# Performance work log

Hardware: AMD Instinct MI355X
Metric: run time of the kernel (lower is better)

Reference implementation:

```python
import jax, jax.numpy as jnp
import numpy as np

NUM_HEADS = 32
HEAD_DIM = 128
NUM_KV_HEADS = 8
SCALE = 0.08838834764831845  # 1/sqrt(128)
SEQ_LEN = 2048
TOTAL_TOKENS = 4096  # batch=2 sequences of 2048


def setup_inputs() -> dict:
    key = jax.random.key(0)
    kq, kk, kv = jax.random.split(key, 3)
    q = jax.random.normal(kq, (TOTAL_TOKENS, NUM_HEADS * HEAD_DIM), dtype=jnp.float32)
    k = jax.random.normal(kk, (TOTAL_TOKENS, NUM_KV_HEADS * HEAD_DIM), dtype=jnp.float32)
    v = jax.random.normal(kv, (TOTAL_TOKENS, NUM_KV_HEADS * HEAD_DIM), dtype=jnp.float32)
    return {"q": q, "k": k, "v": v, "seq_len": SEQ_LEN}


def reference(q, k, v, seq_len):
    # Unified (varlen) causal GQA attention: flattened tokens are split into
    # batch sequences of equal length (the prefill path of the unified kernel).
    T = q.shape[0]
    B = T // seq_len
    G = NUM_HEADS // NUM_KV_HEADS  # query heads per kv head
    # [B, S, Hkv, G, D] and [B, S, Hkv, D]
    qh = q.reshape(B, seq_len, NUM_KV_HEADS, G, HEAD_DIM)
    kh = k.reshape(B, seq_len, NUM_KV_HEADS, HEAD_DIM)
    vh = v.reshape(B, seq_len, NUM_KV_HEADS, HEAD_DIM)
    # scores: [B, Hkv, G, Sq, Sk]
    scores = jnp.einsum("bqhgd,bkhd->bhgqk", qh, kh) * SCALE
    causal = jnp.tril(jnp.ones((seq_len, seq_len), dtype=bool))
    scores = jnp.where(causal, scores, jnp.finfo(scores.dtype).min)
    probs = jax.nn.softmax(scores, axis=-1)
    # out: [B, Sq, Hkv, G, D]
    o = jnp.einsum("bhgqk,bkhd->bqhgd", probs, vh)
    return o.reshape(T, NUM_HEADS * HEAD_DIM)
```

## Files before the change

kernel.cpp:

```cpp
#include <hip/hip_runtime.h>
#include <stdint.h>
#include <stddef.h>


#define S_LEN   2048
#define HQ      32
#define HKV     8
#define DH      128
#define QSTRIDE (HQ*DH)
#define KSTRIDE (HKV*DH)
#define SCALE_L2 0.12751139830213113f

#define KTILE      64
#define NTILES     (S_LEN/KTILE)
#define CSTRIDE    520
#define KPART      (16*CSTRIDE)
#define TILE_ELEMS (KPART + 16*CSTRIDE)

typedef __bf16 bf16;
typedef short        s16x4 __attribute__((ext_vector_type(4)));
typedef short        s16x8 __attribute__((ext_vector_type(8)));
typedef float        f32x4 __attribute__((ext_vector_type(4)));
typedef unsigned int u32x2 __attribute__((ext_vector_type(2)));
typedef unsigned int u32x4 __attribute__((ext_vector_type(4)));

__device__ __forceinline__ unsigned int pk2(float a, float b) {
  union { bf16 h[2]; unsigned int u; } x;
  x.h[0] = (bf16)a; x.h[1] = (bf16)b;
  return x.u;
}

__device__ __forceinline__ int koff(int chunk, int key) {
  return chunk*CSTRIDE + key*8;
}
__device__ __forceinline__ int voff(int unit, int d) {
  return KPART + unit*CSTRIDE + d*4;
}

__global__ __launch_bounds__(512, 4)
void attn_fwd(const float* __restrict__ qg, const float* __restrict__ kg,
              const float* __restrict__ vg, float* __restrict__ og) {
  __shared__ bf16 smem[2*TILE_ELEMS];

  const int tid   = threadIdx.x;
  const int lane  = tid & 63;
  const int wave  = tid >> 6;
  const int l15   = lane & 15;
  const int quad  = lane >> 4;
  const int pairp = blockIdx.x;
  const int h     = blockIdx.y;
  const int b     = blockIdx.z;
  const int hkv   = h >> 2;

  const int fk_key = tid >> 3, fk_cg = tid & 7;
  const int fv_u   = tid & 15, fv_dq = tid >> 4;
  float4 fkx[4], fvx[4];

  auto load_regs = [&](int t) {
    const float* kp = kg + (size_t)(b*S_LEN + t*KTILE + fk_key)*KSTRIDE
                         + hkv*DH + fk_cg*16;
#pragma unroll
    for (int i = 0; i < 4; ++i) fkx[i] = ((const float4*)kp)[i];
    const int d0 = fv_dq*4;
#pragma unroll
    for (int j = 0; j < 4; ++j)
      fvx[j] = *(const float4*)(vg + (size_t)(b*S_LEN + t*KTILE + fv_u*4 + j)*KSTRIDE
                                   + hkv*DH + d0);
  };
  auto store_tile = [&](int bi) {
    bf16* kb = smem + bi*TILE_ELEMS;
#pragma unroll
    for (int ii = 0; ii < 2; ++ii) {
      u32x4 w;
      w[0] = pk2(fkx[2*ii].x,   fkx[2*ii].y);   w[1] = pk2(fkx[2*ii].z,   fkx[2*ii].w);
      w[2] = pk2(fkx[2*ii+1].x, fkx[2*ii+1].y); w[3] = pk2(fkx[2*ii+1].z, fkx[2*ii+1].w);
      *(u32x4*)(kb + koff(fk_cg*2 + ii, fk_key)) = w;
    }
    const float* g0 = (const float*)&fvx[0];
    const float* g1 = (const float*)&fvx[1];
    const float* g2 = (const float*)&fvx[2];
    const float* g3 = (const float*)&fvx[3];
#pragma unroll
    for (int i = 0; i < 4; i += 2) {
      u32x4 w;
      w[0] = pk2(g0[i],   g1[i]);
      w[1] = pk2(g2[i],   g3[i]);
      w[2] = pk2(g0[i+1], g1[i+1]);
      w[3] = pk2(g2[i+1], g3[i+1]);
      *(u32x4*)(kb + voff(fv_u, fv_dq*4 + i)) = w;
    }
  };

  f32x4 oacc[8];
  float m_run, l_run;
  u32x4 qf[4];

  const int qbs[2] = { pairp, 15 - pairp };
  load_regs(0);

  int gs = 0;
#pragma unroll 1
  for (int item = 0; item < 2; ++item) {
    const int qblk = qbs[item];
    const int qw   = qblk*128 + wave*16;
    const int nst  = qblk*2 + 2;

    {
      const float* qp = qg + (size_t)(b*S_LEN + qw + l15)*QSTRIDE
                           + h*DH + quad*8;
#pragma unroll
      for (int c = 0; c < 4; ++c) {
        const float4 a4 = ((const float4*)(qp + c*32))[0];
        const float4 b4 = ((const float4*)(qp + c*32))[1];
        u32x4 w;
        w[0] = pk2(a4.x*SCALE_L2, a4.y*SCALE_L2);
        w[1] = pk2(a4.z*SCALE_L2, a4.w*SCALE_L2);
        w[2] = pk2(b4.x*SCALE_L2, b4.y*SCALE_L2);
        w[3] = pk2(b4.z*SCALE_L2, b4.w*SCALE_L2);
        qf[c] = w;
      }
    }
#pragma unroll
    for (int nd = 0; nd < 8; ++nd) oacc[nd] = (f32x4){0.f, 0.f, 0.f, 0.f};
    m_run = -3e38f; l_run = 0.f;

#pragma unroll 1
    for (int i = 0; i < nst; ++i, ++gs) {
      const int k0  = i*KTILE;
      const int buf = gs & 1;
      store_tile(buf);
      __syncthreads();
      const bool more  = (i + 1 < nst);
      const bool cross = (!more) && (item == 0);
      if (more)       load_regs(i + 1);
      else if (cross) load_regs(0);

      if (k0 <= qw + 15) {
        const bf16* kb = smem + buf*TILE_ELEMS;

        f32x4 sacc[4];
#pragma unroll
        for (int mt = 0; mt < 4; ++mt) sacc[mt] = (f32x4){0.f, 0.f, 0.f, 0.f};
#pragma unroll
        for (int c = 0; c < 4; ++c) {
#pragma unroll
          for (int mt = 0; mt < 4; ++mt) {
            const u32x4 af = *(const u32x4*)(kb + koff(c*4 + quad, mt*16 + l15));
            sacc[mt] = __builtin_amdgcn_mfma_f32_16x16x32_bf16(
                __builtin_bit_cast(s16x8, af), __builtin_bit_cast(s16x8, qf[c]),
                sacc[mt], 0, 0, 0);
          }
        }

        const bool needmask = (k0 + KTILE - 1 > qw);
        const int  qgl = qw + l15;
        float tmax = -3e38f;
#pragma unroll
        for (int mt = 0; mt < 4; ++mt)
#pragma unroll
          for (int r = 0; r < 4; ++r) {
            float sv = sacc[mt][r];
            if (needmask) {
              const int key = k0 + mt*16 + quad*4 + r;
              sv = (key <= qgl) ? sv : -3e38f;
            }
            sacc[mt][r] = sv;
            tmax = fmaxf(tmax, sv);
          }
        tmax = fmaxf(tmax, __shfl_xor(tmax, 16));
        tmax = fmaxf(tmax, __shfl_xor(tmax, 32));
        const float mnew  = fmaxf(m_run, tmax);
        const float alpha = __builtin_amdgcn_exp2f(m_run - mnew);
        m_run = mnew;
        float rsum = 0.f;
#pragma unroll
        for (int mt = 0; mt < 4; ++mt)
#pragma unroll
          for (int r = 0; r < 4; ++r) {
            const float e = __builtin_amdgcn_exp2f(sacc[mt][r] - mnew);
            sacc[mt][r] = e;
            rsum += e;
          }
        rsum += __shfl_xor(rsum, 16);
        rsum += __shfl_xor(rsum, 32);
        l_run = l_run*alpha + rsum;

        s16x4 pa[4];
#pragma unroll
        for (int mt = 0; mt < 4; ++mt) {
          union { bf16 hh[4]; s16x4 s; } u;
#pragma unroll
          for (int r = 0; r < 4; ++r) u.hh[r] = (bf16)sacc[mt][r];
          pa[mt] = u.s;
        }

#pragma unroll
        for (int r = 0; r < 4; ++r) {
          const float a = __shfl(alpha, (lane & 48) | (quad*4 + r));
#pragma unroll
          for (int nd = 0; nd < 8; ++nd) oacc[nd][r] *= a;
        }

#pragma unroll
        for (int kt = 0; kt < 4; ++kt)
#pragma unroll
          for (int nd = 0; nd < 8; ++nd) {
            const s16x4 bv = *(const s16x4*)(kb + voff(kt*4 + quad, nd*16 + l15));
            oacc[nd] = __builtin_amdgcn_mfma_f32_16x16x16bf16_1k(
                pa[kt], bv, oacc[nd], 0, 0, 0);
          }
      }
    }

#pragma unroll
    for (int r = 0; r < 4; ++r) {
      const float li  = __shfl(l_run, (lane & 48) | (quad*4 + r));
      const float inv = 1.0f / li;
      const size_t base = (size_t)(b*S_LEN + qw + quad*4 + r)*QSTRIDE
                        + h*DH + l15;
#pragma unroll
      for (int nd = 0; nd < 8; ++nd)
        og[base + nd*16] = oacc[nd][r] * inv;
    }
  }
}

extern "C" void kernel_launch(void* const* d_in, const int* in_sizes, int n_in,
                              void* d_out, int out_size, void* d_ws, size_t ws_size,
                              hipStream_t stream) {
  const float* q = (const float*)d_in[0];
  const float* k = (const float*)d_in[1];
  const float* v = (const float*)d_in[2];
  float* out = (float*)d_out;
  (void)d_ws; (void)ws_size;
  dim3 grid(8, HQ, 2);
  dim3 block(512);
  attn_fwd<<<grid, block, 0, stream>>>(q, k, v, out);
}
```

Before: 272.1 us.

## Defer online-softmax rescale with wave-uniform threshold and tree reductions

Adds a lazy rescaling rule to the online softmax. When no row's tile max exceeds the running max by more than a threshold (checked wave-wide), the kernel skips the alpha computation, the shuffles and the rescale of the output accumulators. The serial max and sum reductions become balanced trees to shorten the dependency chains. The barrier now comes after the next tile's global loads are issued. The trade-off is that exp2 values can reach up to 2^8 before normalization, which costs some bf16/fp32 headroom, and the vote plus branch adds divergence overhead.

```diff
diff --git a/kernel.cpp b/kernel.cpp
--- a/kernel.cpp
+++ b/kernel.cpp
@@ -10,6 +10,7 @@
 #define QSTRIDE (HQ*DH)
 #define KSTRIDE (HKV*DH)
 #define SCALE_L2 0.12751139830213113f
+#define DEFER_THR 8.0f
 
 #define KTILE      64
 #define NTILES     (S_LEN/KTILE)
@@ -129,11 +130,11 @@
       const int k0  = i*KTILE;
       const int buf = gs & 1;
       store_tile(buf);
-      __syncthreads();
       const bool more  = (i + 1 < nst);
       const bool cross = (!more) && (item == 0);
       if (more)       load_regs(i + 1);
       else if (cross) load_regs(0);
+      __syncthreads();
 
       if (k0 <= qw + 15) {
         const bf16* kb = smem + buf*TILE_ELEMS;
@@ -154,36 +155,66 @@
 
         const bool needmask = (k0 + KTILE - 1 > qw);
         const int  qgl = qw + l15;
-        float tmax = -3e38f;
-#pragma unroll
-        for (int mt = 0; mt < 4; ++mt)
-#pragma unroll
-          for (int r = 0; r < 4; ++r) {
-            float sv = sacc[mt][r];
-            if (needmask) {
+        if (needmask) {
+#pragma unroll
+          for (int mt = 0; mt < 4; ++mt)
+#pragma unroll
+            for (int r = 0; r < 4; ++r) {
               const int key = k0 + mt*16 + quad*4 + r;
-              sv = (key <= qgl) ? sv : -3e38f;
+              if (key > qgl) sacc[mt][r] = -3e38f;
             }
-            sacc[mt][r] = sv;
-            tmax = fmaxf(tmax, sv);
-          }
+        }
+        float tmax;
+        {
+          float t8[8];
+#pragma unroll
+          for (int j = 0; j < 8; ++j)
+            t8[j] = fmaxf(sacc[j >> 2][j & 3], sacc[(j >> 2) + 2][j & 3]);
+          float t4[4];
+#pragma unroll
+          for (int j = 0; j < 4; ++j) t4[j] = fmaxf(t8[j], t8[j + 4]);
+          tmax = fmaxf(fmaxf(t4[0], t4[2]), fmaxf(t4[1], t4[3]));
+        }
         tmax = fmaxf(tmax, __shfl_xor(tmax, 16));
         tmax = fmaxf(tmax, __shfl_xor(tmax, 32));
-        const float mnew  = fmaxf(m_run, tmax);
-        const float alpha = __builtin_amdgcn_exp2f(m_run - mnew);
-        m_run = mnew;
-        float rsum = 0.f;
+
+        const bool defer = __all(tmax <= m_run + DEFER_THR);
+        float alpha = 1.0f;
+        if (!defer) {
+          const float mnew = fmaxf(m_run, tmax);
+          alpha = __builtin_amdgcn_exp2f(m_run - mnew);
+          m_run = mnew;
+        }
 #pragma unroll
         for (int mt = 0; mt < 4; ++mt)
 #pragma unroll
-          for (int r = 0; r < 4; ++r) {
-            const float e = __builtin_amdgcn_exp2f(sacc[mt][r] - mnew);
-            sacc[mt][r] = e;
-            rsum += e;
-          }
+          for (int r = 0; r < 4; ++r)
+            sacc[mt][r] = __builtin_amdgcn_exp2f(sacc[mt][r] - m_run);
+        float rsum;
+        {
+          float s8[8];
+#pragma unroll
+          for (int j = 0; j < 8; ++j)
+            s8[j] = sacc[j >> 2][j & 3] + sacc[(j >> 2) + 2][j & 3];
+          float s4[4];
+#pragma unroll
+          for (int j = 0; j < 4; ++j) s4[j] = s8[j] + s8[j + 4];
+          rsum = (s4[0] + s4[2]) + (s4[1] + s4[3]);
+        }
         rsum += __shfl_xor(rsum, 16);
         rsum += __shfl_xor(rsum, 32);
-        l_run = l_run*alpha + rsum;
+
+        if (defer) {
+          l_run += rsum;
+        } else {
+          l_run = l_run*alpha + rsum;
+#pragma unroll
+          for (int r = 0; r < 4; ++r) {
+            const float a = __shfl(alpha, (lane & 48) | (quad*4 + r));
+#pragma unroll
+            for (int nd = 0; nd < 8; ++nd) oacc[nd][r] *= a;
+          }
+        }
 
         s16x4 pa[4];
 #pragma unroll
@@ -192,13 +223,6 @@
 #pragma unroll
           for (int r = 0; r < 4; ++r) u.hh[r] = (bf16)sacc[mt][r];
           pa[mt] = u.s;
-        }
-
-#pragma unroll
-        for (int r = 0; r < 4; ++r) {
-          const float a = __shfl(alpha, (lane & 48) | (quad*4 + r));
-#pragma unroll
-          for (int nd = 0; nd < 8; ++nd) oacc[nd][r] *= a;
         }
 
 #pragma unroll
```

Result: faster. 257.5 us (-5.4%).
